# Kernel tuning notes

Hardware: AMD Instinct MI355X
Metric: run time of the kernel (lower is better)

Reference implementation:

```python
import jax, jax.numpy as jnp
import numpy as np

B, S, D, E, K, O = 32, 2048, 1024, 16, 4, 1024


def setup_inputs() -> dict:
    key = jax.random.key(0)
    ks = jax.random.split(key, 9)
    sc = 0.02
    return {
        "x": jax.random.normal(ks[0], (B, S, D), dtype=jnp.float32),
        "Wg": jax.random.normal(ks[1], (D, E), dtype=jnp.float32) * sc,
        "bg": jnp.zeros((E,), dtype=jnp.float32),
        "W1": jax.random.normal(ks[2], (E, K * D, O), dtype=jnp.float32) * sc,
        "b1": jnp.zeros((E, O), dtype=jnp.float32),
        "W2": jax.random.normal(ks[3], (E, O, O), dtype=jnp.float32) * sc,
        "b2": jnp.zeros((E, O), dtype=jnp.float32),
        "W3": jax.random.normal(ks[4], (E, O, O), dtype=jnp.float32) * sc,
        "b3": jnp.zeros((E, O), dtype=jnp.float32),
    }


def reference(x, Wg, bg, W1, b1, W2, b2, W3, b3):
    b, s, d = x.shape
    e = Wg.shape[1]
    k = W1.shape[1] // d
    # gate logits [B,S,E]; softmax over the TOKEN axis (dim=-2 in torch)
    logits = jnp.einsum('bsd,de->bse', x, Wg) + bg
    probs = jax.nn.softmax(logits, axis=-2)          # [B,S,E]
    # top-k tokens per expert (torch.topk over dim=-2)
    vals, idx = jax.lax.top_k(probs.transpose(0, 2, 1), k)  # [B,E,k]
    # gather selected tokens: [B,E,k,D]
    tok = jnp.take_along_axis(x[:, None, :, :], idx[..., None], axis=2)
    # weight by gate prob, concat k tokens -> [B,E,k*D]
    inp = (tok * vals[..., None]).reshape(b, e, k * d)
    # per-expert 3-layer MLP as grouped GEMMs
    h = jax.nn.relu(jnp.einsum('bei,eio->beo', inp, W1) + b1)
    h = jax.nn.relu(jnp.einsum('beo,eop->bep', h, W2) + b2)
    out = jnp.einsum('beo,eop->bep', h, W3) + b3
    return out  # [B,E,O]
```

## Files before the change

### kernel.cpp

```cpp
#include <hip/hip_runtime.h>
#include <hip/hip_bf16.h>
#include <math.h>

constexpr int B = 32, S = 2048, D = 1024, E = 16, TK = 4, O = 1024;
constexpr int KD = TK * D;
constexpr int KS = 8;

__global__ __launch_bounds__(256) void k_logits(
    const float* __restrict__ x, const float* __restrict__ Wg,
    const float* __restrict__ bg, float* __restrict__ logitsT) {
  int tid = threadIdx.x;
  int lane = tid & 63;
  int wid = __builtin_amdgcn_readfirstlane(tid >> 6);
  int row0 = blockIdx.x * 64;
  int row = row0 + lane;
  const float* xr = x + (size_t)row * D + wid * 256;
  const float* wg = Wg + (size_t)wid * 256 * E;
  float acc[E];
#pragma unroll
  for (int e = 0; e < E; e++) acc[e] = 0.f;
  for (int it = 0; it < 64; it += 8) {
    float4 xv[8];
#pragma unroll
    for (int u = 0; u < 8; u++)
      xv[u] = *(const float4*)(xr + (it + u) * 4);
#pragma unroll
    for (int u = 0; u < 8; u++) {
      const float* w0 = wg + (size_t)(it + u) * 4 * E;
#pragma unroll
      for (int e = 0; e < E; e++)
        acc[e] += xv[u].x * w0[e] + xv[u].y * w0[E + e] +
                  xv[u].z * w0[2 * E + e] + xv[u].w * w0[3 * E + e];
    }
  }
  __shared__ float red[4][64][17];
#pragma unroll
  for (int e = 0; e < E; e++) red[wid][lane][e] = acc[e];
  __syncthreads();
  int b = row0 >> 11;
  int s0 = row0 & (S - 1);
#pragma unroll
  for (int i = 0; i < 4; i++) {
    int e = wid + i * 4;
    float v = red[0][lane][e] + red[1][lane][e] + red[2][lane][e] +
              red[3][lane][e] + bg[e];
    logitsT[((size_t)b * E + e) * S + s0 + lane] = v;
  }
}

__global__ __launch_bounds__(256) void k_topk(
    const float* __restrict__ logitsT, int* __restrict__ tIdx,
    float* __restrict__ tVal) {
  int be = blockIdx.x;
  const float* lrow = logitsT + (size_t)be * S;
  __shared__ float sv[S];
  __shared__ float red[256];
  __shared__ int redi[256];
  int t = threadIdx.x;
  for (int i = t; i < S; i += 256) sv[i] = lrow[i];
  __syncthreads();
  float m = -1e30f;
  for (int i = t; i < S; i += 256) m = fmaxf(m, sv[i]);
  red[t] = m;
  __syncthreads();
  for (int off = 128; off > 0; off >>= 1) {
    if (t < off) red[t] = fmaxf(red[t], red[t + off]);
    __syncthreads();
  }
  float gmax = red[0];
  __syncthreads();
  float se = 0.f;
  for (int i = t; i < S; i += 256) se += expf(sv[i] - gmax);
  red[t] = se;
  __syncthreads();
  for (int off = 128; off > 0; off >>= 1) {
    if (t < off) red[t] += red[t + off];
    __syncthreads();
  }
  float sumexp = red[0];
  __syncthreads();
  for (int j = 0; j < 4; j++) {
    float bv = -1e30f;
    int bi = S;
    for (int i = t; i < S; i += 256) {
      float v = sv[i];
      if (v > bv || (v == bv && i < bi)) { bv = v; bi = i; }
    }
    red[t] = bv;
    redi[t] = bi;
    __syncthreads();
    for (int off = 128; off > 0; off >>= 1) {
      if (t < off) {
        float v2 = red[t + off];
        int i2 = redi[t + off];
        if (v2 > red[t] || (v2 == red[t] && i2 < redi[t])) {
          red[t] = v2;
          redi[t] = i2;
        }
      }
      __syncthreads();
    }
    if (t == 0) {
      tIdx[be * TK + j] = redi[0];
      tVal[be * TK + j] = expf(red[0] - gmax) / sumexp;
      sv[redi[0]] = -1e30f;
    }
    __syncthreads();
  }
}

__global__ __launch_bounds__(256) void k_gather(
    const float* __restrict__ x, const int* __restrict__ tIdx,
    const float* __restrict__ tVal, float* __restrict__ inpT) {
  int ej = blockIdx.x;
  int e = ej / TK, j = ej % TK;
  int d0 = blockIdx.y * 256;
  __shared__ float st[32][257];
  int tid = threadIdx.x;
  int dt = tid % 64;
  int bq = tid / 64;
  for (int bi = 0; bi < 8; bi++) {
    int b = bq * 8 + bi;
    int row = tIdx[(b * E + e) * TK + j];
    float v = tVal[(b * E + e) * TK + j];
    float4 xv = *(const float4*)(x + ((size_t)b * S + row) * D + d0 + dt * 4);
    st[b][dt * 4 + 0] = xv.x * v;
    st[b][dt * 4 + 1] = xv.y * v;
    st[b][dt * 4 + 2] = xv.z * v;
    st[b][dt * 4 + 3] = xv.w * v;
  }
  __syncthreads();
  size_t base = ((size_t)e * TK + j) * D + d0;
  for (int c = 0; c < 32; c++) {
    int idx = c * 256 + tid;
    int drel = idx / 32, b = idx % 32;
    inpT[(base + drel) * 32 + b] = st[b][drel];
  }
}

template <int KC>
__global__ __launch_bounds__(256) void k_gemm_part(
    const float* __restrict__ AT,
    const float* __restrict__ W,
    float* __restrict__ part,
    int Ktot) {
  int e = blockIdx.x, nt = blockIdx.y, ks = blockIdx.z;
  int tid = threadIdx.x;
  int lane = tid & 63;
  int m0 = __builtin_amdgcn_readfirstlane((tid >> 6) * 8);
  int n0 = nt * 256 + lane * 4;
  int k0 = ks * KC;
  const float* a = AT + ((size_t)e * Ktot + k0) * 32 + m0;
  const float* w = W + ((size_t)e * Ktot + k0) * O + n0;
  float acc[8][4];
#pragma unroll
  for (int m = 0; m < 8; m++)
#pragma unroll
    for (int q = 0; q < 4; q++) acc[m][q] = 0.f;
  for (int k = 0; k < KC; k += 8) {
    float4 wv[8];
#pragma unroll
    for (int u = 0; u < 8; u++)
      wv[u] = *(const float4*)(w + (size_t)(k + u) * O);
#pragma unroll
    for (int u = 0; u < 8; u++) {
      const float* ar = a + (size_t)(k + u) * 32;
#pragma unroll
      for (int m = 0; m < 8; m++) {
        float av = ar[m];
        acc[m][0] += av * wv[u].x;
        acc[m][1] += av * wv[u].y;
        acc[m][2] += av * wv[u].z;
        acc[m][3] += av * wv[u].w;
      }
    }
  }
  float* pb = part + (((size_t)ks * E + e) * O + n0) * 32 + m0;
#pragma unroll
  for (int ni = 0; ni < 4; ni++) {
    *(float4*)(pb + ni * 32) =
        make_float4(acc[0][ni], acc[1][ni], acc[2][ni], acc[3][ni]);
    *(float4*)(pb + ni * 32 + 4) =
        make_float4(acc[4][ni], acc[5][ni], acc[6][ni], acc[7][ni]);
  }
}

__global__ __launch_bounds__(256) void k_reduce_act(
    const float* __restrict__ part, const float* __restrict__ bias,
    float* __restrict__ outT, int relu) {
  size_t g = (size_t)blockIdx.x * 256 + threadIdx.x;
  const size_t stride4 = (size_t)E * O * 32 / 4;
  const float4* p4 = (const float4*)part;
  float4 s = p4[g];
#pragma unroll
  for (int ks = 1; ks < KS; ks++) {
    float4 v = p4[(size_t)ks * stride4 + g];
    s.x += v.x; s.y += v.y; s.z += v.z; s.w += v.w;
  }
  size_t el = g * 4;
  int n = (int)((el / 32) % O);
  int e = (int)(el / ((size_t)32 * O));
  float bv = bias[e * O + n];
  s.x += bv; s.y += bv; s.z += bv; s.w += bv;
  if (relu) {
    s.x = fmaxf(s.x, 0.f); s.y = fmaxf(s.y, 0.f);
    s.z = fmaxf(s.z, 0.f); s.w = fmaxf(s.w, 0.f);
  }
  ((float4*)outT)[g] = s;
}

__global__ __launch_bounds__(256) void k_final(
    const float* __restrict__ part, const float* __restrict__ bias,
    float* __restrict__ out) {
  int e = blockIdx.x;
  int o0 = blockIdx.y * 64;
  __shared__ float sd[64][33];
  int tid = threadIdx.x;
  const size_t stride = (size_t)E * O * 32;
  for (int c = 0; c < 8; c++) {
    int idx = c * 256 + tid;
    int orel = idx / 32, b = idx % 32;
    size_t off = ((size_t)e * O + o0 + orel) * 32 + b;
    float s = part[off];
#pragma unroll
    for (int ks = 1; ks < KS; ks++) s += part[(size_t)ks * stride + off];
    sd[orel][b] = s + bias[e * O + o0 + orel];
  }
  __syncthreads();
  for (int c = 0; c < 8; c++) {
    int idx = c * 256 + tid;
    int b = idx / 64, orr = idx % 64;
    out[((size_t)b * E + e) * O + o0 + orr] = sd[orr][b];
  }
}

extern "C" void kernel_launch(void* const* d_in, const int* in_sizes, int n_in,
                              void* d_out, int out_size, void* d_ws,
                              size_t ws_size, hipStream_t stream) {
  (void)in_sizes; (void)n_in; (void)out_size; (void)ws_size;
  const float* x  = (const float*)d_in[0];
  const float* Wg = (const float*)d_in[1];
  const float* bg = (const float*)d_in[2];
  const float* W1 = (const float*)d_in[3];
  const float* b1 = (const float*)d_in[4];
  const float* W2 = (const float*)d_in[5];
  const float* b2 = (const float*)d_in[6];
  const float* W3 = (const float*)d_in[7];
  const float* b3 = (const float*)d_in[8];
  float* out = (float*)d_out;

  char* ws = (char*)d_ws;
  float* logitsT = (float*)ws;
  int*   tIdx    = (int*)(ws + (4u << 20));
  float* tVal    = (float*)(ws + (4u << 20) + (8u << 10));
  float* inpT    = (float*)(ws + (4u << 20) + (64u << 10));
  float* part    = (float*)(ws + (12u << 20) + (64u << 10));
  float* h1T     = (float*)(ws + (28u << 20) + (64u << 10));
  float* h2T     = (float*)(ws + (30u << 20) + (64u << 10));

  k_logits<<<B * S / 64, 256, 0, stream>>>(x, Wg, bg, logitsT);
  k_topk<<<B * E, 256, 0, stream>>>(logitsT, tIdx, tVal);
  k_gather<<<dim3(E * TK, D / 256), 256, 0, stream>>>(x, tIdx, tVal, inpT);
  k_gemm_part<KD / KS><<<dim3(E, O / 256, KS), 256, 0, stream>>>(inpT, W1, part, KD);
  k_reduce_act<<<(E * O * 32 / 4) / 256, 256, 0, stream>>>(part, b1, h1T, 1);
  k_gemm_part<O / KS><<<dim3(E, O / 256, KS), 256, 0, stream>>>(h1T, W2, part, O);
  k_reduce_act<<<(E * O * 32 / 4) / 256, 256, 0, stream>>>(part, b2, h2T, 1);
  k_gemm_part<O / KS><<<dim3(E, O / 256, KS), 256, 0, stream>>>(h2T, W3, part, O);
  k_final<<<dim3(E, O / 64), 256, 0, stream>>>(part, b3, out);
}
```

Before: 765.1 us.

## Fuse token gather into first expert GEMM and use 512-thread GEMM blocks

Removes the separate gather/transpose kernel and its intermediate buffer. The first GEMM now reads the selected token rows of x directly and applies the gate probability as a scale on the output. All GEMM kernels move to 512 threads with 4 rows per wave instead of 8, doubling the number of waves per block. In exchange, the per-lane reads of x rows are scalar and strided, and each block now has to stream more W traffic.

```diff
diff --git a/kernel.cpp b/kernel.cpp
--- a/kernel.cpp
+++ b/kernel.cpp
@@ -109,37 +109,60 @@
   }
 }
 
-__global__ __launch_bounds__(256) void k_gather(
+__global__ __launch_bounds__(512) void k_gemm1(
     const float* __restrict__ x, const int* __restrict__ tIdx,
-    const float* __restrict__ tVal, float* __restrict__ inpT) {
-  int ej = blockIdx.x;
-  int e = ej / TK, j = ej % TK;
-  int d0 = blockIdx.y * 256;
-  __shared__ float st[32][257];
-  int tid = threadIdx.x;
-  int dt = tid % 64;
-  int bq = tid / 64;
-  for (int bi = 0; bi < 8; bi++) {
-    int b = bq * 8 + bi;
-    int row = tIdx[(b * E + e) * TK + j];
-    float v = tVal[(b * E + e) * TK + j];
-    float4 xv = *(const float4*)(x + ((size_t)b * S + row) * D + d0 + dt * 4);
-    st[b][dt * 4 + 0] = xv.x * v;
-    st[b][dt * 4 + 1] = xv.y * v;
-    st[b][dt * 4 + 2] = xv.z * v;
-    st[b][dt * 4 + 3] = xv.w * v;
-  }
-  __syncthreads();
-  size_t base = ((size_t)e * TK + j) * D + d0;
-  for (int c = 0; c < 32; c++) {
-    int idx = c * 256 + tid;
-    int drel = idx / 32, b = idx % 32;
-    inpT[(base + drel) * 32 + b] = st[b][drel];
-  }
+    const float* __restrict__ tVal, const float* __restrict__ W,
+    float* __restrict__ part) {
+  int e = blockIdx.x, nt = blockIdx.y, ks = blockIdx.z;
+  int tid = threadIdx.x;
+  int lane = tid & 63;
+  int m0 = __builtin_amdgcn_readfirstlane((tid >> 6) * 4);
+  int n0 = nt * 256 + lane * 4;
+  int j = ks >> 1;
+  int d0 = (ks & 1) * 512;
+  int k0 = ks * 512;
+  const float* xb[4];
+  float vm[4];
+#pragma unroll
+  for (int i = 0; i < 4; i++) {
+    int b = m0 + i;
+    int r = tIdx[(b * E + e) * TK + j];
+    vm[i] = tVal[(b * E + e) * TK + j];
+    xb[i] = x + ((size_t)b * S + r) * D + d0;
+  }
+  const float* w = W + ((size_t)e * KD + k0) * O + n0;
+  float acc[4][4];
+#pragma unroll
+  for (int i = 0; i < 4; i++)
+#pragma unroll
+    for (int q = 0; q < 4; q++) acc[i][q] = 0.f;
+  for (int k = 0; k < 512; k += 8) {
+    float4 wv[8];
+#pragma unroll
+    for (int u = 0; u < 8; u++)
+      wv[u] = *(const float4*)(w + (size_t)(k + u) * O);
+#pragma unroll
+    for (int u = 0; u < 8; u++) {
+#pragma unroll
+      for (int i = 0; i < 4; i++) {
+        float av = xb[i][k + u];
+        acc[i][0] += av * wv[u].x;
+        acc[i][1] += av * wv[u].y;
+        acc[i][2] += av * wv[u].z;
+        acc[i][3] += av * wv[u].w;
+      }
+    }
+  }
+  float* pb = part + (((size_t)ks * E + e) * O + n0) * 32 + m0;
+#pragma unroll
+  for (int ni = 0; ni < 4; ni++)
+    *(float4*)(pb + ni * 32) =
+        make_float4(acc[0][ni] * vm[0], acc[1][ni] * vm[1],
+                    acc[2][ni] * vm[2], acc[3][ni] * vm[3]);
 }
 
 template <int KC>
-__global__ __launch_bounds__(256) void k_gemm_part(
+__global__ __launch_bounds__(512) void k_gemm_part(
     const float* __restrict__ AT,
     const float* __restrict__ W,
     float* __restrict__ part,
@@ -147,16 +170,16 @@
   int e = blockIdx.x, nt = blockIdx.y, ks = blockIdx.z;
   int tid = threadIdx.x;
   int lane = tid & 63;
-  int m0 = __builtin_amdgcn_readfirstlane((tid >> 6) * 8);
+  int m0 = __builtin_amdgcn_readfirstlane((tid >> 6) * 4);
   int n0 = nt * 256 + lane * 4;
   int k0 = ks * KC;
   const float* a = AT + ((size_t)e * Ktot + k0) * 32 + m0;
   const float* w = W + ((size_t)e * Ktot + k0) * O + n0;
-  float acc[8][4];
-#pragma unroll
-  for (int m = 0; m < 8; m++)
-#pragma unroll
-    for (int q = 0; q < 4; q++) acc[m][q] = 0.f;
+  float acc[4][4];
+#pragma unroll
+  for (int i = 0; i < 4; i++)
+#pragma unroll
+    for (int q = 0; q < 4; q++) acc[i][q] = 0.f;
   for (int k = 0; k < KC; k += 8) {
     float4 wv[8];
 #pragma unroll
@@ -166,23 +189,20 @@
     for (int u = 0; u < 8; u++) {
       const float* ar = a + (size_t)(k + u) * 32;
 #pragma unroll
-      for (int m = 0; m < 8; m++) {
-        float av = ar[m];
-        acc[m][0] += av * wv[u].x;
-        acc[m][1] += av * wv[u].y;
-        acc[m][2] += av * wv[u].z;
-        acc[m][3] += av * wv[u].w;
+      for (int i = 0; i < 4; i++) {
+        float av = ar[i];
+        acc[i][0] += av * wv[u].x;
+        acc[i][1] += av * wv[u].y;
+        acc[i][2] += av * wv[u].z;
+        acc[i][3] += av * wv[u].w;
       }
     }
   }
   float* pb = part + (((size_t)ks * E + e) * O + n0) * 32 + m0;
 #pragma unroll
-  for (int ni = 0; ni < 4; ni++) {
+  for (int ni = 0; ni < 4; ni++)
     *(float4*)(pb + ni * 32) =
         make_float4(acc[0][ni], acc[1][ni], acc[2][ni], acc[3][ni]);
-    *(float4*)(pb + ni * 32 + 4) =
-        make_float4(acc[4][ni], acc[5][ni], acc[6][ni], acc[7][ni]);
-  }
 }
 
 __global__ __launch_bounds__(256) void k_reduce_act(
@@ -253,18 +273,16 @@
   float* logitsT = (float*)ws;
   int*   tIdx    = (int*)(ws + (4u << 20));
   float* tVal    = (float*)(ws + (4u << 20) + (8u << 10));
-  float* inpT    = (float*)(ws + (4u << 20) + (64u << 10));
   float* part    = (float*)(ws + (12u << 20) + (64u << 10));
   float* h1T     = (float*)(ws + (28u << 20) + (64u << 10));
   float* h2T     = (float*)(ws + (30u << 20) + (64u << 10));
 
   k_logits<<<B * S / 64, 256, 0, stream>>>(x, Wg, bg, logitsT);
   k_topk<<<B * E, 256, 0, stream>>>(logitsT, tIdx, tVal);
-  k_gather<<<dim3(E * TK, D / 256), 256, 0, stream>>>(x, tIdx, tVal, inpT);
-  k_gemm_part<KD / KS><<<dim3(E, O / 256, KS), 256, 0, stream>>>(inpT, W1, part, KD);
+  k_gemm1<<<dim3(E, O / 256, KS), 512, 0, stream>>>(x, tIdx, tVal, W1, part);
   k_reduce_act<<<(E * O * 32 / 4) / 256, 256, 0, stream>>>(part, b1, h1T, 1);
-  k_gemm_part<O / KS><<<dim3(E, O / 256, KS), 256, 0, stream>>>(h1T, W2, part, O);
+  k_gemm_part<O / KS><<<dim3(E, O / 256, KS), 512, 0, stream>>>(h1T, W2, part, O);
   k_reduce_act<<<(E * O * 32 / 4) / 256, 256, 0, stream>>>(part, b2, h2T, 1);
-  k_gemm_part<O / KS><<<dim3(E, O / 256, KS), 256, 0, stream>>>(h2T, W3, part, O);
+  k_gemm_part<O / KS><<<dim3(E, O / 256, KS), 512, 0, stream>>>(h2T, W3, part, O);
   k_final<<<dim3(E, O / 64), 256, 0, stream>>>(part, b3, out);
 }
```

New measurement: 776.4 us. No clear change (+1.5%).
